# Kernel optimization log

Hardware: AMD Instinct MI355X
Metric: run time of the kernel (lower is better)

The kernel has to match this reference:

```python
import jax, jax.numpy as jnp
import numpy as np

EPS = 1e-5

def conv1d(x, w, b, pad):
    # x: [B,C_in,S], w: [C_out,C_in,K] -> [B,C_out,S]
    y = jax.lax.conv_general_dilated(x, w, window_strides=(1,), padding=[(pad, pad)],
                                     dimension_numbers=('NCH', 'OIH', 'NCH'))
    return y + b[None, :, None]

def bn(x, gamma, beta, mean, var):
    # inference-mode BatchNorm1d over channel dim of [B,C,S]
    scale = gamma * jax.lax.rsqrt(var + EPS)
    shift = beta - mean * scale
    return x * scale[None, :, None] + shift[None, :, None]

def setup_inputs() -> dict:
    key = jax.random.key(0)
    ks = jax.random.split(key, 16)
    B, S, D, C, K = 32, 2048, 128, 256, 5
    x = jax.random.normal(ks[0], (B, S, D), dtype=jnp.float32)
    start_padding_indices = jax.random.randint(ks[1], (B,), 0, S, dtype=jnp.int64 if jax.config.jax_enable_x64 else jnp.int32)
    def conv_init(k, co, ci, kk):
        fan = ci * kk
        return jax.random.normal(k, (co, ci, kk), dtype=jnp.float32) / np.sqrt(fan)
    W1 = conv_init(ks[2], C, D, K); b1 = jnp.zeros((C,), jnp.float32)
    g1 = jnp.ones((C,), jnp.float32); be1 = jnp.zeros((C,), jnp.float32)
    m1 = jax.random.normal(ks[3], (C,), dtype=jnp.float32) * 0.1
    v1 = jax.random.uniform(ks[4], (C,), dtype=jnp.float32, minval=0.5, maxval=1.5)
    W2 = conv_init(ks[5], C, C, K); b2 = jnp.zeros((C,), jnp.float32)
    g2 = jnp.ones((C,), jnp.float32); be2 = jnp.zeros((C,), jnp.float32)
    m2 = jax.random.normal(ks[6], (C,), dtype=jnp.float32) * 0.1
    v2 = jax.random.uniform(ks[7], (C,), dtype=jnp.float32, minval=0.5, maxval=1.5)
    Wf = conv_init(ks[8], D, C, 1); bf = jnp.zeros((D,), jnp.float32)
    return {"x": x, "start_padding_indices": start_padding_indices,
            "W1": W1, "b1": b1, "g1": g1, "be1": be1, "m1": m1, "v1": v1,
            "W2": W2, "b2": b2, "g2": g2, "be2": be2, "m2": m2, "v2": v2,
            "Wf": Wf, "bf": bf}

def reference(x, start_padding_indices, W1, b1, g1, be1, m1, v1,
              W2, b2, g2, be2, m2, v2, Wf, bf):
    B, S, D = x.shape
    K = W1.shape[-1]
    h = jnp.transpose(x, (0, 2, 1))                      # [B,D,S]
    h = jax.nn.relu(bn(conv1d(h, W1, b1, K // 2), g1, be1, m1, v1))
    h = jax.nn.relu(bn(conv1d(h, W2, b2, K // 2), g2, be2, m2, v2))
    h = conv1d(h, Wf, bf, 0)                             # [B,D,S]
    conv_out = jnp.transpose(h, (0, 2, 1))               # [B,S,D]
    # vectorized masked mean: -1 sentinel -> full length; 0 -> zeros
    lengths = jnp.where(start_padding_indices == -1, S, start_padding_indices)  # [B]
    mask = jnp.arange(S)[None, :] < lengths[:, None]     # [B,S]
    sums = jnp.sum(conv_out * mask[:, :, None].astype(conv_out.dtype), axis=1)  # [B,D]
    denom = jnp.maximum(lengths, 1).astype(conv_out.dtype)[:, None]
    pooled = jnp.where(lengths[:, None] > 0, sums / denom, jnp.zeros_like(sums))
    return pooled
```

## Files before the change

kernel.cpp:

```cpp
#include <hip/hip_runtime.h>

#define S_LEN 2048
#define NBATCH 32

typedef __bf16 bf16x8 __attribute__((ext_vector_type(8)));
typedef float f32x4 __attribute__((ext_vector_type(4)));
typedef unsigned short bf_t;

__device__ __forceinline__ unsigned short f2bf(float f) {
  __bf16 h = (__bf16)f;
  return __builtin_bit_cast(unsigned short, h);
}

#if __has_builtin(__builtin_amdgcn_global_load_lds)
#define USE_GLL 1
#else
#define USE_GLL 0
#endif

__device__ __forceinline__ void load_lds16(const void* g, void* ldsbase) {
#if USE_GLL
  __builtin_amdgcn_global_load_lds(
      (const __attribute__((address_space(1))) unsigned int*)g,
      (__attribute__((address_space(3))) unsigned int*)ldsbase, 16, 0, 0);
#else
  *(int4*)((char*)ldsbase + (threadIdx.x & 63) * 16) =
      *(const int4*)((const char*)g);
#endif
}

#define WAITV10 asm volatile("s_waitcnt vmcnt(10)" ::: "memory")
#define WAITV8  asm volatile("s_waitcnt vmcnt(8)" ::: "memory")
#define WAITV4  asm volatile("s_waitcnt vmcnt(4)" ::: "memory")
#define WAITV0  asm volatile("s_waitcnt vmcnt(0)" ::: "memory")
#define LGKM0   asm volatile("s_waitcnt lgkmcnt(0)" ::: "memory")

__global__ void convert_x(const float* __restrict__ x, bf_t* __restrict__ xb) {
  const size_t i = (size_t)blockIdx.x * blockDim.x + threadIdx.x;
  const float4 a = ((const float4*)x)[2 * i];
  const float4 c = ((const float4*)x)[2 * i + 1];
  ushort4 o0; o0.x = f2bf(a.x); o0.y = f2bf(a.y); o0.z = f2bf(a.z); o0.w = f2bf(a.w);
  ushort4 o1; o1.x = f2bf(c.x); o1.y = f2bf(c.y); o1.z = f2bf(c.z); o1.w = f2bf(c.w);
  ((ushort4*)xb)[2 * i] = o0;
  ((ushort4*)xb)[2 * i + 1] = o1;
}

__global__ void fold_bn(const float* __restrict__ b1, const float* __restrict__ g1,
                        const float* __restrict__ be1, const float* __restrict__ m1,
                        const float* __restrict__ v1,
                        const float* __restrict__ b2, const float* __restrict__ g2,
                        const float* __restrict__ be2, const float* __restrict__ m2,
                        const float* __restrict__ v2, float* __restrict__ abuf,
                        float* __restrict__ zp) {
  int c = threadIdx.x;
  if (c < 64) zp[c] = 0.f;
  if (c < 256) {
    float a1 = g1[c] * rsqrtf(v1[c] + 1e-5f);
    abuf[c] = a1;
    abuf[256 + c] = (b1[c] - m1[c]) * a1 + be1[c];
    float a2 = g2[c] * rsqrtf(v2[c] + 1e-5f);
    abuf[512 + c] = a2;
    abuf[768 + c] = (b2[c] - m2[c]) * a2 + be2[c];
  }
}

template <int CIN, int TAPS>
__global__ void prep_w2(const float* __restrict__ w, bf_t* __restrict__ wfm) {
  const int idx = blockIdx.x * 256 + threadIdx.x;
  constexpr int total = 256 * CIN * TAPS;
  if (idx >= total) return;
  const int j = idx & 7;
  const int l = (idx >> 3) & 63;
  const int f = (idx >> 9) & 7;
  const int wr = (idx >> 12) & 1;
  const int tg = idx >> 13;
  const int co = wr * 128 + f * 16 + (l & 15);
  const int cc = tg / (TAPS * 4);
  const int k = (tg / 4) % TAPS;
  const int q = tg & 3;
  const int ci = cc * 128 + q * 32 + (l >> 4) * 8 + j;
  wfm[idx] = f2bf(w[((size_t)co * CIN + ci) * TAPS + k]);
}

template <int CIN, int COUT, int TAPS>
__global__ void prep_w(const float* __restrict__ w, bf_t* __restrict__ wfm) {
  constexpr int T = CIN * TAPS / 32;
  const int idx = blockIdx.x * 256 + threadIdx.x;
  constexpr int total = COUT * CIN * TAPS;
  if (idx >= total) return;
  const int j = idx & 7;
  const int l = (idx >> 3) & 63;
  const int f = (idx >> 9) & 3;
  const int gt = idx >> 11;
  const int t = gt % T;
  const int g = gt / T;
  const int co = g * 64 + f * 16 + (l & 15);
  const int cc = t / (TAPS * 4);
  const int k = (t / 4) % TAPS;
  const int q = t & 3;
  const int ci = cc * 128 + q * 32 + (l >> 4) * 8 + j;
  wfm[idx] = f2bf(w[((size_t)co * CIN + ci) * TAPS + k]);
}

template <int CIN, int TAPS>
__global__ __launch_bounds__(512, 2)
void conv_gemm(const bf_t* __restrict__ xin, const bf_t* __restrict__ wfm,
               const float* __restrict__ alpha, const float* __restrict__ bias,
               const float* __restrict__ zp, bf_t* __restrict__ hout) {
  constexpr int HALO = (TAPS - 1) / 2;
  constexpr int P = (CIN / 128) * TAPS * 4;
  constexpr int NKT = P / 2;

  __shared__ char smem[131072];

  const int tid = threadIdx.x;
  const int l = tid & 63;
  const int wv = tid >> 6;
  const int wr = wv >> 2;
  const int wn = wv & 3;
  const int b = blockIdx.x >> 3;
  const int s0 = (blockIdx.x & 7) << 8;
  const int l15 = l & 15;
  const int l4 = l >> 4;
  const int wu16 = (tid - l) * 16;

  f32x4 acc[8][4] = {};

  auto STAGE_A = [&](int t) {
    const char* src = (const char*)wfm + (size_t)t * 16384;
    char* dst = smem + ((t >> 1) & 1) * 32768 + (t & 1) * 16384;
    load_lds16(src + tid * 16, dst + wu16);
    load_lds16(src + 8192 + tid * 16, dst + 8192 + wu16);
  };

  auto STAGE_B = [&](int j, int sub) {
    const int t = 2 * j + sub;
    const int cc = t / (TAPS * 4);
    const int k = (t >> 2) % TAPS;
    const int q = t & 3;
    char* dst = smem + 65536 + (j & 1) * 32768 + sub * 16384;
    const char* srcb = (const char*)xin +
        ((size_t)b * S_LEN * CIN + cc * 128 + q * 32) * 2 + (tid & 3) * 16;
    const int r0 = tid >> 2;
    {
      const int s = s0 + r0 - HALO + k;
      const char* src = ((unsigned)s < (unsigned)S_LEN)
          ? srcb + (size_t)s * (CIN * 2) : (const char*)zp;
      load_lds16(src, dst + wu16);
    }
    {
      const int s = s0 + r0 + 128 - HALO + k;
      const char* src = ((unsigned)s < (unsigned)S_LEN)
          ? srcb + (size_t)s * (CIN * 2) : (const char*)zp;
      load_lds16(src, dst + 8192 + wu16);
    }
  };

  STAGE_A(0); STAGE_B(0, 0); STAGE_A(1); STAGE_B(0, 1);
  STAGE_A(2); STAGE_B(1, 0); STAGE_A(3);
  WAITV10;
  __builtin_amdgcn_s_barrier();

#pragma unroll 1
  for (int j = 0; j < NKT; ++j) {
    const char* Ab = smem + (j & 1) * 32768;
    const char* Bb = smem + 65536 + (j & 1) * 32768;
    bf16x8 afr[8], bfr0, bfr1;

#pragma unroll
    for (int f = 0; f < 8; ++f)
      afr[f] = *(const bf16x8*)(Ab + wr * 8192 + f * 1024 + l * 16);
    bfr0 = *(const bf16x8*)(Bb + (wn * 64 + 0 + l15) * 64 + l4 * 16);
    bfr1 = *(const bf16x8*)(Bb + (wn * 64 + 16 + l15) * 64 + l4 * 16);
    if (j + 1 < NKT) STAGE_B(j + 1, 1);
    __builtin_amdgcn_s_barrier();
    LGKM0; __builtin_amdgcn_sched_barrier(0);
    __builtin_amdgcn_s_setprio(1);
#pragma unroll
    for (int f = 0; f < 8; ++f) {
      acc[f][0] = __builtin_amdgcn_mfma_f32_16x16x32_bf16(afr[f], bfr0, acc[f][0], 0, 0, 0);
      acc[f][1] = __builtin_amdgcn_mfma_f32_16x16x32_bf16(afr[f], bfr1, acc[f][1], 0, 0, 0);
    }
    __builtin_amdgcn_s_setprio(0);
    __builtin_amdgcn_s_barrier();

    bfr0 = *(const bf16x8*)(Bb + (wn * 64 + 32 + l15) * 64 + l4 * 16);
    bfr1 = *(const bf16x8*)(Bb + (wn * 64 + 48 + l15) * 64 + l4 * 16);
    if (j + 2 < NKT) STAGE_A(2 * (j + 2));
    __builtin_amdgcn_s_barrier();
    LGKM0; __builtin_amdgcn_sched_barrier(0);
    __builtin_amdgcn_s_setprio(1);
#pragma unroll
    for (int f = 0; f < 8; ++f) {
      acc[f][2] = __builtin_amdgcn_mfma_f32_16x16x32_bf16(afr[f], bfr0, acc[f][2], 0, 0, 0);
      acc[f][3] = __builtin_amdgcn_mfma_f32_16x16x32_bf16(afr[f], bfr1, acc[f][3], 0, 0, 0);
    }
    __builtin_amdgcn_s_setprio(0);
    if (j <= NKT - 3) { WAITV10; } else if (j == NKT - 2) { WAITV8; } else { WAITV0; }
    __builtin_amdgcn_s_barrier();

#pragma unroll
    for (int f = 0; f < 8; ++f)
      afr[f] = *(const bf16x8*)(Ab + 16384 + wr * 8192 + f * 1024 + l * 16);
    bfr0 = *(const bf16x8*)(Bb + 16384 + (wn * 64 + 0 + l15) * 64 + l4 * 16);
    bfr1 = *(const bf16x8*)(Bb + 16384 + (wn * 64 + 16 + l15) * 64 + l4 * 16);
    if (j + 2 < NKT) STAGE_B(j + 2, 0);
    __builtin_amdgcn_s_barrier();
    LGKM0; __builtin_amdgcn_sched_barrier(0);
    __builtin_amdgcn_s_setprio(1);
#pragma unroll
    for (int f = 0; f < 8; ++f) {
      acc[f][0] = __builtin_amdgcn_mfma_f32_16x16x32_bf16(afr[f], bfr0, acc[f][0], 0, 0, 0);
      acc[f][1] = __builtin_amdgcn_mfma_f32_16x16x32_bf16(afr[f], bfr1, acc[f][1], 0, 0, 0);
    }
    __builtin_amdgcn_s_setprio(0);
    __builtin_amdgcn_s_barrier();

    bfr0 = *(const bf16x8*)(Bb + 16384 + (wn * 64 + 32 + l15) * 64 + l4 * 16);
    bfr1 = *(const bf16x8*)(Bb + 16384 + (wn * 64 + 48 + l15) * 64 + l4 * 16);
    if (j + 2 < NKT) STAGE_A(2 * (j + 2) + 1);
    __builtin_amdgcn_s_barrier();
    LGKM0; __builtin_amdgcn_sched_barrier(0);
    __builtin_amdgcn_s_setprio(1);
#pragma unroll
    for (int f = 0; f < 8; ++f) {
      acc[f][2] = __builtin_amdgcn_mfma_f32_16x16x32_bf16(afr[f], bfr0, acc[f][2], 0, 0, 0);
      acc[f][3] = __builtin_amdgcn_mfma_f32_16x16x32_bf16(afr[f], bfr1, acc[f][3], 0, 0, 0);
    }
    __builtin_amdgcn_s_setprio(0);
    if (j + 2 < NKT) { WAITV10; } else if (j + 1 < NKT) { WAITV4; }
    __builtin_amdgcn_s_barrier();
  }

  const int cobase = wr * 128;
#pragma unroll
  for (int f = 0; f < 8; ++f) {
    const int co0 = cobase + f * 16 + l4 * 4;
    const f32x4 al = *(const f32x4*)(alpha + co0);
    const f32x4 bi = *(const f32x4*)(bias + co0);
#pragma unroll
    for (int n = 0; n < 4; ++n) {
      const int sp = wn * 64 + n * 16 + l15;
      ushort4 pk;
      pk.x = f2bf(fmaxf(acc[f][n][0] * al[0] + bi[0], 0.f));
      pk.y = f2bf(fmaxf(acc[f][n][1] * al[1] + bi[1], 0.f));
      pk.z = f2bf(fmaxf(acc[f][n][2] * al[2] + bi[2], 0.f));
      pk.w = f2bf(fmaxf(acc[f][n][3] * al[3] + bi[3], 0.f));
      *(ushort4*)(smem + sp * 512 + ((co0 * 2) ^ ((sp & 7) << 4))) = pk;
    }
  }
  __syncthreads();
  {
    char* hb = (char*)hout + ((size_t)(b * S_LEN + s0) * 256) * 2;
#pragma unroll
    for (int k = 0; k < 16; ++k) {
      const int c = tid + k * 512;
      const int sp = c >> 5;
      const int col = (c & 31) * 16;
      const int4 v = *(const int4*)(smem + sp * 512 + (col ^ ((sp & 7) << 4)));
      *(int4*)(hb + (size_t)sp * 512 + col) = v;
    }
  }
}

__global__ __launch_bounds__(512, 4)
void conv_pool(const bf_t* __restrict__ xin, const bf_t* __restrict__ wfm,
               const float* __restrict__ bfin, const int* __restrict__ spi,
               float* __restrict__ gpart) {
  constexpr int CIN = 256;
  constexpr int T = 8;

  __shared__ char smem[128 * 256];
  __shared__ float red[4][128];

  const int tid = threadIdx.x;
  const int l = tid & 63;
  const int wv = tid >> 6;
  const int wr = wv >> 2;
  const int wn = wv & 3;
  const int nb = blockIdx.x;
  const int b = nb >> 4;
  const int st = nb & 15;
  const int s0 = st << 7;
  const int l15 = l & 15;
  const int l4 = l >> 4;

  f32x4 acc[4][2] = {};
  const bf_t* wbase = wfm + (size_t)wr * (T * 2048);

  for (int cc = 0; cc < 2; ++cc) {
    const char* src = (const char*)xin + ((size_t)b * S_LEN * CIN + cc * 128) * 2;
    for (int off = tid * 16; off < 128 * 256; off += 512 * 16) {
      const int row = off >> 8;
      const int c = off & 255;
      const int cs = c ^ ((row & 7) << 4);
      void* ldsbase = (void*)(smem + (off - l * 16));
      load_lds16(src + (size_t)(s0 + row) * (CIN * 2) + cs, ldsbase);
    }
    __syncthreads();

#pragma unroll
    for (int q = 0; q < 4; ++q) {
      const int t = cc * 4 + q;
      bf16x8 bfr[2];
#pragma unroll
      for (int fn = 0; fn < 2; ++fn) {
        const int row = wn * 32 + fn * 16 + l15;
        const int cb = q * 64 + l4 * 16;
        bfr[fn] = *(const bf16x8*)(smem + row * 256 + (cb ^ ((row & 7) << 4)));
      }
#pragma unroll
      for (int f = 0; f < 4; ++f) {
        const bf16x8 afr =
            *(const bf16x8*)(wbase + ((size_t)(t * 4 + f) * 64 + l) * 8);
        acc[f][0] = __builtin_amdgcn_mfma_f32_16x16x32_bf16(afr, bfr[0], acc[f][0], 0, 0, 0);
        acc[f][1] = __builtin_amdgcn_mfma_f32_16x16x32_bf16(afr, bfr[1], acc[f][1], 0, 0, 0);
      }
    }
    __syncthreads();
  }

  int len = spi[b];
  if (len < 0) len = S_LEN;

#pragma unroll
  for (int f = 0; f < 4; ++f) {
    const int co0 = wr * 64 + f * 16 + l4 * 4;
    const f32x4 bi = *(const f32x4*)(bfin + co0);
    f32x4 vs = {};
#pragma unroll
    for (int fn = 0; fn < 2; ++fn) {
      const int s = s0 + wn * 32 + fn * 16 + l15;
      const float m = (s < len) ? 1.f : 0.f;
      vs[0] += (acc[f][fn][0] + bi[0]) * m;
      vs[1] += (acc[f][fn][1] + bi[1]) * m;
      vs[2] += (acc[f][fn][2] + bi[2]) * m;
      vs[3] += (acc[f][fn][3] + bi[3]) * m;
    }
#pragma unroll
    for (int d = 1; d < 16; d <<= 1) {
      vs[0] += __shfl_xor(vs[0], d, 64);
      vs[1] += __shfl_xor(vs[1], d, 64);
      vs[2] += __shfl_xor(vs[2], d, 64);
      vs[3] += __shfl_xor(vs[3], d, 64);
    }
    if (l15 == 0) {
      red[wn][co0 + 0] = vs[0];
      red[wn][co0 + 1] = vs[1];
      red[wn][co0 + 2] = vs[2];
      red[wn][co0 + 3] = vs[3];
    }
  }
  __syncthreads();
  if (tid < 128) {
    float p = red[0][tid] + red[1][tid] + red[2][tid] + red[3][tid];
    gpart[((size_t)b * 16 + st) * 128 + tid] = p;
  }
}

__global__ void finalize(const float* __restrict__ gpart, const int* __restrict__ spi,
                         float* __restrict__ out) {
  const int b = blockIdx.x;
  const int d = threadIdx.x;
  float s = 0.f;
#pragma unroll
  for (int t = 0; t < 16; ++t) s += gpart[((size_t)b * 16 + t) * 128 + d];
  int len = spi[b];
  if (len < 0) len = S_LEN;
  float denom = (float)(len < 1 ? 1 : len);
  out[b * 128 + d] = s / denom;
}

extern "C" void kernel_launch(void* const* d_in, const int* in_sizes, int n_in,
                              void* d_out, int out_size, void* d_ws, size_t ws_size,
                              hipStream_t stream) {
  (void)in_sizes; (void)n_in; (void)out_size; (void)ws_size;
  const float* x = (const float*)d_in[0];
  const int* spi = (const int*)d_in[1];
  const float* W1 = (const float*)d_in[2];
  const float* b1 = (const float*)d_in[3];
  const float* g1 = (const float*)d_in[4];
  const float* be1 = (const float*)d_in[5];
  const float* m1 = (const float*)d_in[6];
  const float* v1 = (const float*)d_in[7];
  const float* W2 = (const float*)d_in[8];
  const float* b2 = (const float*)d_in[9];
  const float* g2 = (const float*)d_in[10];
  const float* be2 = (const float*)d_in[11];
  const float* m2 = (const float*)d_in[12];
  const float* v2 = (const float*)d_in[13];
  const float* Wf = (const float*)d_in[14];
  const float* bf_ = (const float*)d_in[15];
  float* out = (float*)d_out;

  char* ws = (char*)d_ws;
  float* zp   = (float*)(ws);
  bf_t* xb    = (bf_t*)(ws + 4096);
  bf_t* h1    = (bf_t*)(ws + 16781312);
  bf_t* h2    = (bf_t*)(ws + 50335744);
  bf_t* wf1   = (bf_t*)(ws + 83890176);
  bf_t* wf2   = (bf_t*)(ws + 84217856);
  bf_t* wff   = (bf_t*)(ws + 84873216);
  float* abuf = (float*)(ws + 84938752);
  float* gpart= (float*)(ws + 84942848);

  convert_x<<<4096, 256, 0, stream>>>(x, xb);
  fold_bn<<<1, 256, 0, stream>>>(b1, g1, be1, m1, v1, b2, g2, be2, m2, v2, abuf, zp);
  prep_w2<128, 5><<<640, 256, 0, stream>>>(W1, wf1);
  prep_w2<256, 5><<<1280, 256, 0, stream>>>(W2, wf2);
  prep_w<256, 128, 1><<<128, 256, 0, stream>>>(Wf, wff);

  conv_gemm<128, 5><<<256, 512, 0, stream>>>(xb, wf1, abuf, abuf + 256, zp, h1);
  conv_gemm<256, 5><<<256, 512, 0, stream>>>(h1, wf2, abuf + 512, abuf + 768, zp, h2);
  conv_pool<<<512, 512, 0, stream>>>(h2, wff, bf_, spi, gpart);
  finalize<<<32, 128, 0, stream>>>(gpart, spi, out);
}
```

Baseline: 108.3 us.

## Software-pipeline LDS fragment loads and XOR-swizzle B tile in conv GEMM

Restructures the conv GEMM main loop so the LDS fragment reads for the next MFMA phase are issued before the current MFMA batch, using double-buffered A/B fragment registers. This lets LDS reads overlap matrix compute instead of waiting on lgkmcnt before each phase. It also XOR-swizzles the B tile's 16-byte column slots on both the global-to-LDS copy and the fragment reads to reduce LDS bank conflicts. In exchange, the doubled fragment registers raise register pressure, and the vmcnt wait accounting is simplified to a uniform WAITV8 with a final WAITV0.

```diff
diff --git a/kernel.cpp b/kernel.cpp
--- a/kernel.cpp
+++ b/kernel.cpp
@@ -29,11 +29,8 @@
 #endif
 }
 
-#define WAITV10 asm volatile("s_waitcnt vmcnt(10)" ::: "memory")
 #define WAITV8  asm volatile("s_waitcnt vmcnt(8)" ::: "memory")
-#define WAITV4  asm volatile("s_waitcnt vmcnt(4)" ::: "memory")
 #define WAITV0  asm volatile("s_waitcnt vmcnt(0)" ::: "memory")
-#define LGKM0   asm volatile("s_waitcnt lgkmcnt(0)" ::: "memory")
 
 __global__ void convert_x(const float* __restrict__ x, bf_t* __restrict__ xb) {
   const size_t i = (size_t)blockIdx.x * blockDim.x + threadIdx.x;
@@ -103,10 +100,10 @@
 }
 
 template <int CIN, int TAPS>
-__global__ __launch_bounds__(512, 2)
-void conv_gemm(const bf_t* __restrict__ xin, const bf_t* __restrict__ wfm,
-               const float* __restrict__ alpha, const float* __restrict__ bias,
-               const float* __restrict__ zp, bf_t* __restrict__ hout) {
+__device__ __forceinline__ void conv_body(
+    const bf_t* __restrict__ xin, const bf_t* __restrict__ wfm,
+    const float* __restrict__ alpha, const float* __restrict__ bias,
+    const float* __restrict__ zp, bf_t* __restrict__ hout) {
   constexpr int HALO = (TAPS - 1) / 2;
   constexpr int P = (CIN / 128) * TAPS * 4;
   constexpr int NKT = P / 2;
@@ -125,113 +122,133 @@
   const int wu16 = (tid - l) * 16;
 
   f32x4 acc[8][4] = {};
-
-  auto STAGE_A = [&](int t) {
-    const char* src = (const char*)wfm + (size_t)t * 16384;
-    char* dst = smem + ((t >> 1) & 1) * 32768 + (t & 1) * 16384;
+  bf16x8 afr[2][8];
+  bf16x8 bfr01[2], bfr23[2];
+
+  auto STAGE_A = [&](int jt, int sub) {
+    const char* src = (const char*)wfm + (size_t)(2 * jt + sub) * 16384;
+    char* dst = smem + (jt & 1) * 32768 + sub * 16384;
     load_lds16(src + tid * 16, dst + wu16);
     load_lds16(src + 8192 + tid * 16, dst + 8192 + wu16);
   };
 
-  auto STAGE_B = [&](int j, int sub) {
-    const int t = 2 * j + sub;
+  auto STAGE_B = [&](int jt, int sub) {
+    const int t = 2 * jt + sub;
     const int cc = t / (TAPS * 4);
     const int k = (t >> 2) % TAPS;
     const int q = t & 3;
-    char* dst = smem + 65536 + (j & 1) * 32768 + sub * 16384;
+    char* dst = smem + 65536 + (jt & 1) * 32768 + sub * 16384;
+    const int r0 = tid >> 2;
+    const int slot = ((r0 & 3) ^ ((r0 >> 2) & 3)) << 4;
     const char* srcb = (const char*)xin +
-        ((size_t)b * S_LEN * CIN + cc * 128 + q * 32) * 2 + (tid & 3) * 16;
-    const int r0 = tid >> 2;
+        ((size_t)b * S_LEN * CIN + cc * 128 + q * 32) * 2 +
+        (((tid & 3) * 16) ^ slot);
     {
       const int s = s0 + r0 - HALO + k;
       const char* src = ((unsigned)s < (unsigned)S_LEN)
-          ? srcb + (size_t)s * (CIN * 2) : (const char*)zp;
+          ? srcb + (size_t)s * (CIN * 2) : ((const char*)zp + (((tid & 3) * 16) ^ slot));
       load_lds16(src, dst + wu16);
     }
     {
       const int s = s0 + r0 + 128 - HALO + k;
       const char* src = ((unsigned)s < (unsigned)S_LEN)
-          ? srcb + (size_t)s * (CIN * 2) : (const char*)zp;
+          ? srcb + (size_t)s * (CIN * 2) : ((const char*)zp + (((tid & 3) * 16) ^ slot));
       load_lds16(src, dst + 8192 + wu16);
     }
   };
 
-  STAGE_A(0); STAGE_B(0, 0); STAGE_A(1); STAGE_B(0, 1);
-  STAGE_A(2); STAGE_B(1, 0); STAGE_A(3);
-  WAITV10;
+  auto LDB = [&](const char* Bb, int sub, int r) -> bf16x8 {
+    const int slot = (((r & 3) ^ ((r >> 2) & 3)) << 4);
+    return *(const bf16x8*)(Bb + sub * 16384 + r * 64 + ((l4 * 16) ^ slot));
+  };
+
+  STAGE_A(0, 0); STAGE_B(0, 0); STAGE_A(0, 1); STAGE_B(0, 1);
+  STAGE_A(1, 0); STAGE_B(1, 0); STAGE_A(1, 1);
+  WAITV8;
   __builtin_amdgcn_s_barrier();
+
+  {
+    const char* Ab0 = smem;
+    const char* Bb0 = smem + 65536;
+#pragma unroll
+    for (int f = 0; f < 8; ++f)
+      afr[0][f] = *(const bf16x8*)(Ab0 + wr * 8192 + f * 1024 + l * 16);
+    bfr01[0] = LDB(Bb0, 0, wn * 64 + 0 + l15);
+    bfr01[1] = LDB(Bb0, 0, wn * 64 + 16 + l15);
+  }
 
 #pragma unroll 1
   for (int j = 0; j < NKT; ++j) {
     const char* Ab = smem + (j & 1) * 32768;
     const char* Bb = smem + 65536 + (j & 1) * 32768;
-    bf16x8 afr[8], bfr0, bfr1;
+    const char* Abn = smem + ((j + 1) & 1) * 32768;
+    const char* Bbn = smem + 65536 + ((j + 1) & 1) * 32768;
+
+    bfr23[0] = LDB(Bb, 0, wn * 64 + 32 + l15);
+    bfr23[1] = LDB(Bb, 0, wn * 64 + 48 + l15);
+    if (j + 1 < NKT) STAGE_B(j + 1, 1);
+    __builtin_amdgcn_s_setprio(1);
+#pragma unroll
+    for (int f = 0; f < 8; ++f) {
+      acc[f][0] = __builtin_amdgcn_mfma_f32_16x16x32_bf16(afr[0][f], bfr01[0], acc[f][0], 0, 0, 0);
+      acc[f][1] = __builtin_amdgcn_mfma_f32_16x16x32_bf16(afr[0][f], bfr01[1], acc[f][1], 0, 0, 0);
+    }
+    __builtin_amdgcn_s_setprio(0);
+    WAITV8;
+    __builtin_amdgcn_s_barrier();
+    __builtin_amdgcn_sched_barrier(0);
 
 #pragma unroll
     for (int f = 0; f < 8; ++f)
-      afr[f] = *(const bf16x8*)(Ab + wr * 8192 + f * 1024 + l * 16);
-    bfr0 = *(const bf16x8*)(Bb + (wn * 64 + 0 + l15) * 64 + l4 * 16);
-    bfr1 = *(const bf16x8*)(Bb + (wn * 64 + 16 + l15) * 64 + l4 * 16);
-    if (j + 1 < NKT) STAGE_B(j + 1, 1);
-    __builtin_amdgcn_s_barrier();
-    LGKM0; __builtin_amdgcn_sched_barrier(0);
+      afr[1][f] = *(const bf16x8*)(Ab + 16384 + wr * 8192 + f * 1024 + l * 16);
+    bfr01[0] = LDB(Bb, 1, wn * 64 + 0 + l15);
+    bfr01[1] = LDB(Bb, 1, wn * 64 + 16 + l15);
+    if (j + 2 < NKT) STAGE_A(j + 2, 0);
     __builtin_amdgcn_s_setprio(1);
 #pragma unroll
     for (int f = 0; f < 8; ++f) {
-      acc[f][0] = __builtin_amdgcn_mfma_f32_16x16x32_bf16(afr[f], bfr0, acc[f][0], 0, 0, 0);
-      acc[f][1] = __builtin_amdgcn_mfma_f32_16x16x32_bf16(afr[f], bfr1, acc[f][1], 0, 0, 0);
+      acc[f][2] = __builtin_amdgcn_mfma_f32_16x16x32_bf16(afr[0][f], bfr23[0], acc[f][2], 0, 0, 0);
+      acc[f][3] = __builtin_amdgcn_mfma_f32_16x16x32_bf16(afr[0][f], bfr23[1], acc[f][3], 0, 0, 0);
     }
     __builtin_amdgcn_s_setprio(0);
     __builtin_amdgcn_s_barrier();
-
-    bfr0 = *(const bf16x8*)(Bb + (wn * 64 + 32 + l15) * 64 + l4 * 16);
-    bfr1 = *(const bf16x8*)(Bb + (wn * 64 + 48 + l15) * 64 + l4 * 16);
-    if (j + 2 < NKT) STAGE_A(2 * (j + 2));
+    __builtin_amdgcn_sched_barrier(0);
+
+    bfr23[0] = LDB(Bb, 1, wn * 64 + 32 + l15);
+    bfr23[1] = LDB(Bb, 1, wn * 64 + 48 + l15);
+    if (j + 2 < NKT) STAGE_B(j + 2, 0);
+    __builtin_amdgcn_s_setprio(1);
+#pragma unroll
+    for (int f = 0; f < 8; ++f) {
+      acc[f][0] = __builtin_amdgcn_mfma_f32_16x16x32_bf16(afr[1][f], bfr01[0], acc[f][0], 0, 0, 0);
+      acc[f][1] = __builtin_amdgcn_mfma_f32_16x16x32_bf16(afr[1][f], bfr01[1], acc[f][1], 0, 0, 0);
+    }
+    __builtin_amdgcn_s_setprio(0);
+    WAITV8;
     __builtin_amdgcn_s_barrier();
-    LGKM0; __builtin_amdgcn_sched_barrier(0);
+    __builtin_amdgcn_sched_barrier(0);
+
+    if (j + 1 < NKT) {
+#pragma unroll
+      for (int f = 0; f < 8; ++f)
+        afr[0][f] = *(const bf16x8*)(Abn + wr * 8192 + f * 1024 + l * 16);
+      bfr01[0] = LDB(Bbn, 0, wn * 64 + 0 + l15);
+      bfr01[1] = LDB(Bbn, 0, wn * 64 + 16 + l15);
+    }
+    if (j + 2 < NKT) STAGE_A(j + 2, 1);
     __builtin_amdgcn_s_setprio(1);
 #pragma unroll
     for (int f = 0; f < 8; ++f) {
-      acc[f][2] = __builtin_amdgcn_mfma_f32_16x16x32_bf16(afr[f], bfr0, acc[f][2], 0, 0, 0);
-      acc[f][3] = __builtin_amdgcn_mfma_f32_16x16x32_bf16(afr[f], bfr1, acc[f][3], 0, 0, 0);
-    }
-    __builtin_amdgcn_s_setprio(0);
-    if (j <= NKT - 3) { WAITV10; } else if (j == NKT - 2) { WAITV8; } else { WAITV0; }
-    __builtin_amdgcn_s_barrier();
-
-#pragma unroll
-    for (int f = 0; f < 8; ++f)
-      afr[f] = *(const bf16x8*)(Ab + 16384 + wr * 8192 + f * 1024 + l * 16);
-    bfr0 = *(const bf16x8*)(Bb + 16384 + (wn * 64 + 0 + l15) * 64 + l4 * 16);
-    bfr1 = *(const bf16x8*)(Bb + 16384 + (wn * 64 + 16 + l15) * 64 + l4 * 16);
-    if (j + 2 < NKT) STAGE_B(j + 2, 0);
-    __builtin_amdgcn_s_barrier();
-    LGKM0; __builtin_amdgcn_sched_barrier(0);
-    __builtin_amdgcn_s_setprio(1);
-#pragma unroll
-    for (int f = 0; f < 8; ++f) {
-      acc[f][0] = __builtin_amdgcn_mfma_f32_16x16x32_bf16(afr[f], bfr0, acc[f][0], 0, 0, 0);
-      acc[f][1] = __builtin_amdgcn_mfma_f32_16x16x32_bf16(afr[f], bfr1, acc[f][1], 0, 0, 0);
+      acc[f][2] = __builtin_amdgcn_mfma_f32_16x16x32_bf16(afr[1][f], bfr23[0], acc[f][2], 0, 0, 0);
+      acc[f][3] = __builtin_amdgcn_mfma_f32_16x16x32_bf16(afr[1][f], bfr23[1], acc[f][3], 0, 0, 0);
     }
     __builtin_amdgcn_s_setprio(0);
     __builtin_amdgcn_s_barrier();
-
-    bfr0 = *(const bf16x8*)(Bb + 16384 + (wn * 64 + 32 + l15) * 64 + l4 * 16);
-    bfr1 = *(const bf16x8*)(Bb + 16384 + (wn * 64 + 48 + l15) * 64 + l4 * 16);
-    if (j + 2 < NKT) STAGE_A(2 * (j + 2) + 1);
-    __builtin_amdgcn_s_barrier();
-    LGKM0; __builtin_amdgcn_sched_barrier(0);
-    __builtin_amdgcn_s_setprio(1);
-#pragma unroll
-    for (int f = 0; f < 8; ++f) {
-      acc[f][2] = __builtin_amdgcn_mfma_f32_16x16x32_bf16(afr[f], bfr0, acc[f][2], 0, 0, 0);
-      acc[f][3] = __builtin_amdgcn_mfma_f32_16x16x32_bf16(afr[f], bfr1, acc[f][3], 0, 0, 0);
-    }
-    __builtin_amdgcn_s_setprio(0);
-    if (j + 2 < NKT) { WAITV10; } else if (j + 1 < NKT) { WAITV4; }
-    __builtin_amdgcn_s_barrier();
-  }
-
+    __builtin_amdgcn_sched_barrier(0);
+  }
+
+  WAITV0;
+  __syncthreads();
   const int cobase = wr * 128;
 #pragma unroll
   for (int f = 0; f < 8; ++f) {
@@ -261,6 +278,20 @@
       *(int4*)(hb + (size_t)sp * 512 + col) = v;
     }
   }
+}
+
+__global__ __launch_bounds__(512, 2)
+void conv_gemm_L1(const bf_t* __restrict__ xin, const bf_t* __restrict__ wfm,
+                  const float* __restrict__ alpha, const float* __restrict__ bias,
+                  const float* __restrict__ zp, bf_t* __restrict__ hout) {
+  conv_body<128, 5>(xin, wfm, alpha, bias, zp, hout);
+}
+
+__global__ __launch_bounds__(512, 2)
+void conv_gemm_L2(const bf_t* __restrict__ xin, const bf_t* __restrict__ wfm,
+                  const float* __restrict__ alpha, const float* __restrict__ bias,
+                  const float* __restrict__ zp, bf_t* __restrict__ hout) {
+  conv_body<256, 5>(xin, wfm, alpha, bias, zp, hout);
 }
 
 __global__ __launch_bounds__(512, 4)
@@ -410,8 +441,8 @@
   prep_w2<256, 5><<<1280, 256, 0, stream>>>(W2, wf2);
   prep_w<256, 128, 1><<<128, 256, 0, stream>>>(Wf, wff);
 
-  conv_gemm<128, 5><<<256, 512, 0, stream>>>(xb, wf1, abuf, abuf + 256, zp, h1);
-  conv_gemm<256, 5><<<256, 512, 0, stream>>>(h1, wf2, abuf + 512, abuf + 768, zp, h2);
+  conv_gemm_L1<<<256, 512, 0, stream>>>(xb, wf1, abuf, abuf + 256, zp, h1);
+  conv_gemm_L2<<<256, 512, 0, stream>>>(h1, wf2, abuf + 512, abuf + 768, zp, h2);
   conv_pool<<<512, 512, 0, stream>>>(h2, wff, bf_, spi, gpart);
   finalize<<<32, 128, 0, stream>>>(gpart, spi, out);
 }
```

New measurement: 104.2 us. 1.04x faster.
